# Kernel tuning notes

Hardware: AMD Instinct MI355X
Metric: run time of the kernel (lower is better)

The kernel has to match this reference:

```python
import jax, jax.numpy as jnp
import numpy as np

G = 64        # number of graphs in the batch
NPER = 128    # nodes per graph (equal-size segments -> static shapes)
F = 256       # node feature dim
RATIO = 0.5
K_KEEP = int(np.ceil(RATIO * NPER))  # nodes kept per graph = 64
N = G * NPER


def setup_inputs() -> dict:
    key = jax.random.key(0)
    kx, ka, kk = jax.random.split(key, 3)
    X = jax.random.normal(kx, (N, F), dtype=jnp.float32)
    A = (jax.random.uniform(ka, (N, N)) < 0.01).astype(jnp.float32)
    # segment ids: graph id per node, contiguous equal-size segments
    I = (jnp.arange(N, dtype=jnp.int32) // NPER).astype(jnp.int32)
    kernel = jax.random.normal(kk, (F, 1), dtype=jnp.float32) * 0.05
    return {"X": X, "A": A, "I": I, "kernel": kernel}


def reference(X, A, I, kernel):
    # y = GNN score: A @ (X @ kernel), shape (N, 1)
    y = A @ (X @ kernel)
    scores = y[:, 0]

    # segment-wise top-k (equal-size segments -> reshape instead of padded scatter)
    dense_y = scores.reshape(G, NPER)                 # (G, NPER)
    perm = jnp.argsort(-dense_y, axis=1)              # descending per graph
    idx = perm[:, :K_KEEP] + (jnp.arange(G) * NPER)[:, None]
    # tf.boolean_mask keeps original node order -> sort selected indices
    idx = jnp.sort(idx.reshape(-1))                   # (G*K_KEEP,)

    # gated features, then gather pooled nodes
    features = X * jnp.tanh(y)                        # (N, F)
    X_pooled = features[idx]                          # (G*K_KEEP, F)

    # A^2 for connectivity, then gather rows+cols
    A_squared = A @ A                                 # (N, N)
    A_pooled = A_squared[idx][:, idx]                 # (G*K_KEEP, G*K_KEEP)

    I_pooled = I[idx]                                 # (G*K_KEEP,)
    return X_pooled, A_pooled, I_pooled
```

## Files before the change

kernel.cpp:

```cpp
#include <hip/hip_runtime.h>
#include <cmath>

#define N_    8192
#define F_    256
#define G_    64
#define NPER_ 128
#define KK_   64
#define M_    4096
#define NZCAP 256

__global__ __launch_bounds__(256) void k_xk(const float* __restrict__ X,
                                            const float* __restrict__ ker,
                                            float* __restrict__ Xk) {
    int wave = threadIdx.x >> 6, lane = threadIdx.x & 63;
    int row  = blockIdx.x * 4 + wave;
    const float4* xr = (const float4*)(X + (size_t)row * F_);
    const float4* kr = (const float4*)ker;
    float4 a = xr[lane], b = kr[lane];
    float v = a.x*b.x + a.y*b.y + a.z*b.z + a.w*b.w;
    for (int off = 32; off; off >>= 1) v += __shfl_down(v, off);
    if (lane == 0) Xk[row] = v;
}

__global__ __launch_bounds__(256) void k_y(const float* __restrict__ A,
                                           const float* __restrict__ Xk,
                                           float* __restrict__ y,
                                           unsigned long long* __restrict__ Afw) {
    int wave = threadIdx.x >> 6, lane = threadIdx.x & 63;
    int row  = blockIdx.x * 4 + wave;
    const float4* ar = (const float4*)(A + (size_t)row * N_);
    const float4* xr = (const float4*)Xk;
    unsigned long long* out = Afw + (size_t)row * 128;
    float v = 0.f;
#pragma unroll 4
    for (int t = 0; t < 32; ++t) {
        float4 a = ar[lane + 64*t];
        float4 b = xr[lane + 64*t];
        v += a.x*b.x + a.y*b.y + a.z*b.z + a.w*b.w;
        unsigned long long b0 = __ballot(a.x != 0.f);
        unsigned long long b1 = __ballot(a.y != 0.f);
        unsigned long long b2 = __ballot(a.z != 0.f);
        unsigned long long b3 = __ballot(a.w != 0.f);
        if (lane == 0) {
            out[t*4+0] = b0; out[t*4+1] = b1;
            out[t*4+2] = b2; out[t*4+3] = b3;
        }
    }
    for (int off = 32; off; off >>= 1) v += __shfl_down(v, off);
    if (lane == 0) y[row] = v;
}

__global__ void k_select(const float* __restrict__ y,
                         int* __restrict__ idx) {
    __shared__ float s[NPER_];
    __shared__ unsigned char f[NPER_];
    int g = blockIdx.x, t = threadIdx.x;
    float my = y[g*NPER_ + t];
    s[t] = my;
    __syncthreads();
    int rank = 0;
#pragma unroll 8
    for (int u = 0; u < NPER_; ++u) {
        float su = s[u];
        rank += (su > my) || (su == my && u < t);
    }
    int sel = rank < KK_;
    f[t] = (unsigned char)sel;
    __syncthreads();
    int pos = 0;
    for (int u = 0; u < t; ++u) pos += f[u];
    if (sel) idx[g*KK_ + pos] = g*NPER_ + t;
}

__global__ __launch_bounds__(128) void k_nz(const unsigned long long* __restrict__ Afw,
                                            const int* __restrict__ idx,
                                            unsigned short* __restrict__ nzl,
                                            int* __restrict__ nzc) {
    __shared__ int cnt;
    int i = blockIdx.x, t = threadIdx.x;
    if (t == 0) cnt = 0;
    __syncthreads();
    int r = idx[i];
    unsigned long long m = Afw[(size_t)r*128 + t];
    int n = __popcll(m);
    int base = n ? atomicAdd(&cnt, n) : 0;
    int tt = t >> 2, e = t & 3;
    while (m) {
        int l = __builtin_ctzll(m);
        m &= m - 1;
        int k = tt*256 + l*4 + e;
        if (base < NZCAP) nzl[(size_t)i*NZCAP + base] = (unsigned short)k;
        ++base;
    }
    __syncthreads();
    if (t == 0) nzc[i] = cnt > NZCAP ? NZCAP : cnt;
}

__global__ __launch_bounds__(256) void k_bitc(const unsigned long long* __restrict__ Afw,
                                              const int* __restrict__ idx,
                                              unsigned short* __restrict__ Ab) {
    int k = blockIdx.x, t = threadIdx.x;
    const unsigned long long* rw = Afw + (size_t)k*128;
    unsigned m = 0;
#pragma unroll
    for (int b = 0; b < 16; ++b) {
        int c = idx[t*16 + b];
        int w = ((c >> 8) << 2) | (c & 3);
        int l = (c & 255) >> 2;
        m |= (unsigned)((rw[w] >> l) & 1ULL) << b;
    }
    Ab[(size_t)k*256 + t] = (unsigned short)m;
}

__global__ __launch_bounds__(256) void k_spmm(const unsigned short* __restrict__ Ab,
                                              const unsigned short* __restrict__ nzl,
                                              const int* __restrict__ nzc,
                                              float* __restrict__ C) {
    __shared__ unsigned short ks[NZCAP];
    __shared__ int scnt;
    int i = blockIdx.x, t = threadIdx.x;
    if (t == 0) scnt = nzc[i];
    if (t < NZCAP) ks[t] = nzl[(size_t)i*NZCAP + t];
    __syncthreads();
    int cnt = scnt;
    unsigned acc0 = 0, acc1 = 0, acc2 = 0, acc3 = 0;
    unsigned m = cnt > 0 ? (unsigned)Ab[(size_t)ks[0]*256 + t] : 0u;
    for (int q = 0; q < cnt; ++q) {
        unsigned mn = (q + 1 < cnt) ? (unsigned)Ab[(size_t)ks[q+1]*256 + t] : 0u;
        acc0 += ((m        & 0xFu) * 0x204081u) & 0x01010101u;
        acc1 += (((m >> 4) & 0xFu) * 0x204081u) & 0x01010101u;
        acc2 += (((m >> 8) & 0xFu) * 0x204081u) & 0x01010101u;
        acc3 += ((m >> 12)         * 0x204081u) & 0x01010101u;
        m = mn;
    }
    float4* cp = (float4*)(C + (size_t)i * M_ + t*16);
    unsigned a[4] = {acc0, acc1, acc2, acc3};
#pragma unroll
    for (int d = 0; d < 4; ++d)
        cp[d] = (float4){(float)(a[d] & 255u), (float)((a[d] >> 8) & 255u),
                         (float)((a[d] >> 16) & 255u), (float)(a[d] >> 24)};
}

__global__ __launch_bounds__(64) void k_xpool(const float* __restrict__ X,
                                              const float* __restrict__ y,
                                              const int* __restrict__ idx,
                                              const int* __restrict__ Iin,
                                              float* __restrict__ Xp,
                                              float* __restrict__ Ip) {
    int i   = blockIdx.x;
    int src = idx[i];
    float t = tanhf(y[src]);
    const float4* xr = (const float4*)(X + (size_t)src * F_);
    float4* op = (float4*)(Xp + (size_t)i * F_);
    float4 v = xr[threadIdx.x];
    op[threadIdx.x] = (float4){v.x*t, v.y*t, v.z*t, v.w*t};
    if (threadIdx.x == 0) Ip[i] = (float)Iin[src];
}

extern "C" void kernel_launch(void* const* d_in, const int* in_sizes, int n_in,
                              void* d_out, int out_size, void* d_ws, size_t ws_size,
                              hipStream_t stream) {
    const float* X   = (const float*)d_in[0];
    const float* A   = (const float*)d_in[1];
    const int*   Iin = (const int*)d_in[2];
    const float* ker = (const float*)d_in[3];

    float* out = (float*)d_out;
    float* Xp = out;
    float* Ap = out + (size_t)M_ * F_;
    float* Ip = Ap  + (size_t)M_ * M_;

    char* ws = (char*)d_ws;
    unsigned long long* Afw = (unsigned long long*)ws;
    unsigned short* Ab  = (unsigned short*)(ws + (8u<<20));
    unsigned short* nzl = (unsigned short*)(ws + (12u<<20));
    char* tail = ws + (14u<<20);
    int*   nzc = (int*)  (tail);
    float* Xk  = (float*)(tail + 32768);
    float* yv  = (float*)(tail + 65536);
    int*   idx = (int*)  (tail + 98304);

    k_xk    <<<N_/4, 256, 0, stream>>>(X, ker, Xk);
    k_y     <<<N_/4, 256, 0, stream>>>(A, Xk, yv, Afw);
    k_select<<<G_,   128, 0, stream>>>(yv, idx);
    k_nz    <<<M_,   128, 0, stream>>>(Afw, idx, nzl, nzc);
    k_bitc  <<<N_,   256, 0, stream>>>(Afw, idx, Ab);
    k_xpool <<<M_,    64, 0, stream>>>(X, yv, idx, Iin, Xp, Ip);
    k_spmm  <<<M_,   256, 0, stream>>>(Ab, nzl, nzc, Ap);
}
```

Baseline: 473.6 us.

## Fuse post-select kernels, use nontemporal A loads, restructure bit compaction with LDS

Merges the nonzero-list, bit-compaction and X pooling kernels into one launch that dispatches on block index, cutting two launches. Bit compaction now handles 8 rows per block, staging the index-to-word map and the row bitmasks in shared memory so the index array is not reloaded per row. The A read in the score kernel uses nontemporal loads to avoid polluting cache with the 256MB stream, and the spmm loop prefetches two rows ahead. This adds branch heterogeneity within one grid and more LDS use per block.

```diff
diff --git a/kernel.cpp b/kernel.cpp
--- a/kernel.cpp
+++ b/kernel.cpp
@@ -8,6 +8,8 @@
 #define KK_   64
 #define M_    4096
 #define NZCAP 256
+
+typedef __attribute__((ext_vector_type(4))) float nf4;
 
 __global__ __launch_bounds__(256) void k_xk(const float* __restrict__ X,
                                             const float* __restrict__ ker,
@@ -28,13 +30,13 @@
                                            unsigned long long* __restrict__ Afw) {
     int wave = threadIdx.x >> 6, lane = threadIdx.x & 63;
     int row  = blockIdx.x * 4 + wave;
-    const float4* ar = (const float4*)(A + (size_t)row * N_);
+    const nf4* ar = (const nf4*)(A + (size_t)row * N_);
     const float4* xr = (const float4*)Xk;
     unsigned long long* out = Afw + (size_t)row * 128;
     float v = 0.f;
 #pragma unroll 4
     for (int t = 0; t < 32; ++t) {
-        float4 a = ar[lane + 64*t];
+        nf4 a = __builtin_nontemporal_load(&ar[lane + 64*t]);
         float4 b = xr[lane + 64*t];
         v += a.x*b.x + a.y*b.y + a.z*b.z + a.w*b.w;
         unsigned long long b0 = __ballot(a.x != 0.f);
@@ -72,44 +74,79 @@
     if (sel) idx[g*KK_ + pos] = g*NPER_ + t;
 }
 
-__global__ __launch_bounds__(128) void k_nz(const unsigned long long* __restrict__ Afw,
-                                            const int* __restrict__ idx,
-                                            unsigned short* __restrict__ nzl,
-                                            int* __restrict__ nzc) {
-    __shared__ int cnt;
-    int i = blockIdx.x, t = threadIdx.x;
-    if (t == 0) cnt = 0;
-    __syncthreads();
-    int r = idx[i];
-    unsigned long long m = Afw[(size_t)r*128 + t];
-    int n = __popcll(m);
-    int base = n ? atomicAdd(&cnt, n) : 0;
-    int tt = t >> 2, e = t & 3;
-    while (m) {
-        int l = __builtin_ctzll(m);
-        m &= m - 1;
-        int k = tt*256 + l*4 + e;
-        if (base < NZCAP) nzl[(size_t)i*NZCAP + base] = (unsigned short)k;
-        ++base;
-    }
-    __syncthreads();
-    if (t == 0) nzc[i] = cnt > NZCAP ? NZCAP : cnt;
-}
-
-__global__ __launch_bounds__(256) void k_bitc(const unsigned long long* __restrict__ Afw,
+__global__ __launch_bounds__(256) void k_post(const unsigned long long* __restrict__ Afw,
                                               const int* __restrict__ idx,
-                                              unsigned short* __restrict__ Ab) {
-    int k = blockIdx.x, t = threadIdx.x;
-    const unsigned long long* rw = Afw + (size_t)k*128;
-    unsigned m = 0;
-#pragma unroll
-    for (int b = 0; b < 16; ++b) {
-        int c = idx[t*16 + b];
-        int w = ((c >> 8) << 2) | (c & 3);
-        int l = (c & 255) >> 2;
-        m |= (unsigned)((rw[w] >> l) & 1ULL) << b;
-    }
-    Ab[(size_t)k*256 + t] = (unsigned short)m;
+                                              const float* __restrict__ X,
+                                              const float* __restrict__ y,
+                                              const int* __restrict__ Iin,
+                                              unsigned short* __restrict__ nzl,
+                                              int* __restrict__ nzc,
+                                              unsigned short* __restrict__ Ab,
+                                              float* __restrict__ Xp,
+                                              float* __restrict__ Ip) {
+    __shared__ __align__(16) unsigned char smem[16384 + 16];
+    int b = blockIdx.x, t = threadIdx.x;
+
+    if (b < 2048) {
+        int* cnt2 = (int*)smem;
+        int half = t >> 7, tw = t & 127;
+        int i = b*2 + half;
+        if (tw == 0) cnt2[half] = 0;
+        __syncthreads();
+        int r = idx[i];
+        unsigned long long m = Afw[(size_t)r*128 + tw];
+        int n = __popcll(m);
+        int base = n ? atomicAdd(&cnt2[half], n) : 0;
+        int tt = tw >> 2, e = tw & 3;
+        while (m) {
+            int l = __builtin_ctzll(m);
+            m &= m - 1;
+            int k = tt*256 + l*4 + e;
+            if (base < NZCAP) nzl[(size_t)i*NZCAP + base] = (unsigned short)k;
+            ++base;
+        }
+        __syncthreads();
+        if (tw == 0) nzc[i] = cnt2[half] > NZCAP ? NZCAP : cnt2[half];
+    } else if (b < 3072) {
+        unsigned short* wl = (unsigned short*)smem;
+        unsigned long long* rw = (unsigned long long*)(smem + 8192);
+        int kbase = (b - 2048) * 8;
+        for (int j = t; j < 4096; j += 256) {
+            int c = idx[j];
+            wl[j] = (unsigned short)(((((c >> 8) << 2) | (c & 3)) << 6) | ((c & 255) >> 2));
+        }
+        for (int e = t; e < 1024; e += 256)
+            rw[e] = Afw[(size_t)(kbase + (e >> 7)) * 128 + (e & 127)];
+        __syncthreads();
+        unsigned mreg[8] = {0,0,0,0,0,0,0,0};
+        uint4 q0 = *(const uint4*)&wl[t*16];
+        uint4 q1 = *(const uint4*)&wl[t*16 + 8];
+        unsigned qa[8] = {q0.x, q0.y, q0.z, q0.w, q1.x, q1.y, q1.z, q1.w};
+#pragma unroll
+        for (int mpair = 0; mpair < 8; ++mpair) {
+            unsigned pr = qa[mpair];
+            int w0 = (pr & 0xFFFFu) >> 6, l0 = pr & 63;
+            int w1 = (pr >> 22),          l1 = (pr >> 16) & 63;
+#pragma unroll
+            for (int rr = 0; rr < 8; ++rr) {
+                mreg[rr] |= (unsigned)((rw[rr*128 + w0] >> l0) & 1ULL) << (2*mpair);
+                mreg[rr] |= (unsigned)((rw[rr*128 + w1] >> l1) & 1ULL) << (2*mpair + 1);
+            }
+        }
+#pragma unroll
+        for (int rr = 0; rr < 8; ++rr)
+            Ab[(size_t)(kbase + rr)*256 + t] = (unsigned short)mreg[rr];
+    } else {
+        int wave = t >> 6, lane = t & 63;
+        int i = (b - 3072)*4 + wave;
+        int src = idx[i];
+        float tv = tanhf(y[src]);
+        const float4* xr = (const float4*)(X + (size_t)src * F_);
+        float4* op = (float4*)(Xp + (size_t)i * F_);
+        float4 v = xr[lane];
+        op[lane] = (float4){v.x*tv, v.y*tv, v.z*tv, v.w*tv};
+        if (lane == 0) Ip[i] = (float)Iin[src];
+    }
 }
 
 __global__ __launch_bounds__(256) void k_spmm(const unsigned short* __restrict__ Ab,
@@ -124,14 +161,15 @@
     __syncthreads();
     int cnt = scnt;
     unsigned acc0 = 0, acc1 = 0, acc2 = 0, acc3 = 0;
-    unsigned m = cnt > 0 ? (unsigned)Ab[(size_t)ks[0]*256 + t] : 0u;
+    unsigned m0 = cnt > 0 ? (unsigned)Ab[(size_t)ks[0]*256 + t] : 0u;
+    unsigned m1 = cnt > 1 ? (unsigned)Ab[(size_t)ks[1]*256 + t] : 0u;
     for (int q = 0; q < cnt; ++q) {
-        unsigned mn = (q + 1 < cnt) ? (unsigned)Ab[(size_t)ks[q+1]*256 + t] : 0u;
-        acc0 += ((m        & 0xFu) * 0x204081u) & 0x01010101u;
-        acc1 += (((m >> 4) & 0xFu) * 0x204081u) & 0x01010101u;
-        acc2 += (((m >> 8) & 0xFu) * 0x204081u) & 0x01010101u;
-        acc3 += ((m >> 12)         * 0x204081u) & 0x01010101u;
-        m = mn;
+        unsigned mn = (q + 2 < cnt) ? (unsigned)Ab[(size_t)ks[q+2]*256 + t] : 0u;
+        acc0 += ((m0        & 0xFu) * 0x204081u) & 0x01010101u;
+        acc1 += (((m0 >> 4) & 0xFu) * 0x204081u) & 0x01010101u;
+        acc2 += (((m0 >> 8) & 0xFu) * 0x204081u) & 0x01010101u;
+        acc3 += ((m0 >> 12)         * 0x204081u) & 0x01010101u;
+        m0 = m1; m1 = mn;
     }
     float4* cp = (float4*)(C + (size_t)i * M_ + t*16);
     unsigned a[4] = {acc0, acc1, acc2, acc3};
@@ -139,22 +177,6 @@
     for (int d = 0; d < 4; ++d)
         cp[d] = (float4){(float)(a[d] & 255u), (float)((a[d] >> 8) & 255u),
                          (float)((a[d] >> 16) & 255u), (float)(a[d] >> 24)};
-}
-
-__global__ __launch_bounds__(64) void k_xpool(const float* __restrict__ X,
-                                              const float* __restrict__ y,
-                                              const int* __restrict__ idx,
-                                              const int* __restrict__ Iin,
-                                              float* __restrict__ Xp,
-                                              float* __restrict__ Ip) {
-    int i   = blockIdx.x;
-    int src = idx[i];
-    float t = tanhf(y[src]);
-    const float4* xr = (const float4*)(X + (size_t)src * F_);
-    float4* op = (float4*)(Xp + (size_t)i * F_);
-    float4 v = xr[threadIdx.x];
-    op[threadIdx.x] = (float4){v.x*t, v.y*t, v.z*t, v.w*t};
-    if (threadIdx.x == 0) Ip[i] = (float)Iin[src];
 }
 
 extern "C" void kernel_launch(void* const* d_in, const int* in_sizes, int n_in,
@@ -183,8 +205,6 @@
     k_xk    <<<N_/4, 256, 0, stream>>>(X, ker, Xk);
     k_y     <<<N_/4, 256, 0, stream>>>(A, Xk, yv, Afw);
     k_select<<<G_,   128, 0, stream>>>(yv, idx);
-    k_nz    <<<M_,   128, 0, stream>>>(Afw, idx, nzl, nzc);
-    k_bitc  <<<N_,   256, 0, stream>>>(Afw, idx, Ab);
-    k_xpool <<<M_,    64, 0, stream>>>(X, yv, idx, Iin, Xp, Ip);
+    k_post  <<<4096, 256, 0, stream>>>(Afw, idx, X, yv, Iin, nzl, nzc, Ab, Xp, Ip);
     k_spmm  <<<M_,   256, 0, stream>>>(Ab, nzl, nzc, Ap);
 }
```

After: 444.0 us. 1.07x faster.
